# Performance work log

Measured on AMD Instinct MI355X. Metric: run time of the kernel, lower is better.

Reference implementation:

```python
import jax, jax.numpy as jnp
import numpy as np

TEMPERATURE = 0.1

def _l2norm(x):
    # F.normalize(dim=1) with eps clamp
    n = jnp.maximum(jnp.linalg.norm(x, axis=1, keepdims=True), 1e-12)
    return x / n

def _retrieval_metric(s):
    # T=1: position of the diagonal element in each row's descending sort.
    order = jnp.argsort(-s, axis=1)            # [N,N] descending argsort
    rankpos = jnp.argsort(order, axis=1)        # inverse permutation: rank of each column
    pos = jnp.diagonal(rankpos)                 # j such that rank[i][j] == i
    posf = pos.astype(s.dtype)
    r1 = jnp.mean((pos < 1).astype(s.dtype))
    r5 = jnp.mean((pos < 5).astype(s.dtype))
    r10 = jnp.mean((pos < 10).astype(s.dtype))
    mr = jnp.mean(posf)
    return r1, r5, r10, mr

def setup_inputs() -> dict:
    key = jax.random.key(0)
    k1, k2, k3, k4 = jax.random.split(key, 4)
    N, C = 4096, 512
    return {
        'v_feat': jax.random.normal(k1, (N, C), dtype=jnp.float32),
        't_feat': jax.random.normal(k2, (N, C), dtype=jnp.float32),
        'p_v': jax.random.normal(k3, (N, C), dtype=jnp.float32),
        'p_t': jax.random.normal(k4, (N, C), dtype=jnp.float32),
    }

def reference(v_feat, t_feat, p_v, p_t):
    vn = _l2norm(v_feat)
    tn = _l2norm(t_feat)
    pvn = _l2norm(p_v)
    ptn = _l2norm(p_t)
    sv = jnp.einsum('nc,mc->nm', vn, ptn) / TEMPERATURE  # [N,N]
    st = jnp.einsum('nc,mc->nm', tn, pvn) / TEMPERATURE  # [N,N]
    # nominator: scalar logsumexp over both diagonals (2N values)
    nominator = jax.nn.logsumexp(jnp.concatenate([jnp.diagonal(sv), jnp.diagonal(st)], axis=0))
    # denominator: per-row logsumexp over concatenated [N,2N]
    denominator = jax.nn.logsumexp(jnp.concatenate([sv, st], axis=1), axis=1)
    loss = jnp.mean(denominator - nominator)
    # metrics (no-grad path in original)
    v_std = jnp.mean(jnp.std(vn, axis=0, ddof=1))
    t_std = jnp.mean(jnp.std(tn, axis=0, ddof=1))
    pv_std = jnp.mean(jnp.std(pvn, axis=0, ddof=1))
    pt_std = jnp.mean(jnp.std(ptn, axis=0, ddof=1))
    sv_raw = jnp.einsum('nc,mc->nm', vn, ptn)
    st_raw = jnp.einsum('nc,mc->nm', tn, pvn)
    v_r1, v_r5, v_r10, v_mr = _retrieval_metric(sv_raw)
    t_r1, t_r5, t_r10, t_mr = _retrieval_metric(st_raw)
    return (loss, v_std, t_std, pv_std, pt_std,
            v_r1, v_r5, v_r10, v_mr,
            t_r1, t_r5, t_r10, t_mr)
```

## Files before the change

kernel.cpp:

```cpp
#include <hip/hip_runtime.h>
#include <hip/hip_bf16.h>

#define N 4096
#define C 512

typedef __attribute__((ext_vector_type(8))) short bf16x8;
typedef __attribute__((ext_vector_type(8))) short s16x8;
typedef __attribute__((ext_vector_type(4))) float f32x4;

__device__ inline float bf2f(__hip_bfloat16 h) { return __bfloat162float(h); }

__device__ inline void gload16(const void* g, void* l) {
    __builtin_amdgcn_global_load_lds(
        (__attribute__((address_space(1))) void*)(g),
        (__attribute__((address_space(3))) void*)(l),
        16, 0, 0);
}

__global__ __launch_bounds__(256) void k_prep(
    const float* __restrict__ s0, const float* __restrict__ s1f,
    const float* __restrict__ s2f, const float* __restrict__ s3,
    __hip_bfloat16* __restrict__ ws_hi0, long mat_stride,
    float* __restrict__ dv, float* __restrict__ dt,
    float* __restrict__ colsum, float* __restrict__ colsq)
{
    __shared__ float sa[4][512];
    __shared__ float sq[4][512];

    const int b = blockIdx.x;
    const int tid = threadIdx.x;
    const int lane = tid & 63;
    const int w = tid >> 6;

    const int pair = b >> 8;
    const int chunk = b & 255;
    const float* X = pair ? s1f : s0;
    const float* B = pair ? s2f : s3;
    const int mX = pair ? 1 : 0;
    const int mB = pair ? 2 : 3;
    __hip_bfloat16* hiX = ws_hi0 + (long)mX * mat_stride;
    __hip_bfloat16* loX = hiX + (long)N * C;
    __hip_bfloat16* hiB = ws_hi0 + (long)mB * mat_stride;
    __hip_bfloat16* loB = hiB + (long)N * C;
    float* dout = pair ? dt : dv;

    float aX[8], qX[8], aB[8], qB[8];
    for (int e = 0; e < 8; e++) { aX[e] = 0.f; qX[e] = 0.f; aB[e] = 0.f; qB[e] = 0.f; }

    const int row0 = chunk * 16 + w * 4;
    for (int i = 0; i < 4; i++) {
        const int row = row0 + i;
        const float4* x4 = (const float4*)(X + (size_t)row * C);
        const float4* b4 = (const float4*)(B + (size_t)row * C);
        float4 x0 = x4[lane * 2], x1 = x4[lane * 2 + 1];
        float4 b0 = b4[lane * 2], b1 = b4[lane * 2 + 1];

        float ss  = x0.x*x0.x + x0.y*x0.y + x0.z*x0.z + x0.w*x0.w
                  + x1.x*x1.x + x1.y*x1.y + x1.z*x1.z + x1.w*x1.w;
        float ssb = b0.x*b0.x + b0.y*b0.y + b0.z*b0.z + b0.w*b0.w
                  + b1.x*b1.x + b1.y*b1.y + b1.z*b1.z + b1.w*b1.w;
        float dot = x0.x*b0.x + x0.y*b0.y + x0.z*b0.z + x0.w*b0.w
                  + x1.x*b1.x + x1.y*b1.y + x1.z*b1.z + x1.w*b1.w;
        for (int o = 1; o < 64; o <<= 1) {
            ss  += __shfl_xor(ss, o);
            ssb += __shfl_xor(ssb, o);
            dot += __shfl_xor(dot, o);
        }
        float scX = 1.0f / fmaxf(sqrtf(ss), 1e-12f);
        float scB = 1.0f / fmaxf(sqrtf(ssb), 1e-12f);
        if (lane == 0) dout[row] = dot * scX * scB;

        float yx[8] = { x0.x*scX, x0.y*scX, x0.z*scX, x0.w*scX,
                        x1.x*scX, x1.y*scX, x1.z*scX, x1.w*scX };
        float yb[8] = { b0.x*scB, b0.y*scB, b0.z*scB, b0.w*scB,
                        b1.x*scB, b1.y*scB, b1.z*scB, b1.w*scB };
        __hip_bfloat16 hvx[8], lvx[8], hvb[8], lvb[8];
        for (int e = 0; e < 8; e++) {
            hvx[e] = __float2bfloat16(yx[e]);
            lvx[e] = __float2bfloat16(yx[e] - bf2f(hvx[e]));
            aX[e] += yx[e]; qX[e] += yx[e] * yx[e];
            hvb[e] = __float2bfloat16(yb[e]);
            lvb[e] = __float2bfloat16(yb[e] - bf2f(hvb[e]));
            aB[e] += yb[e]; qB[e] += yb[e] * yb[e];
        }
        size_t base = (size_t)row * C + lane * 8;
        *(s16x8*)(hiX + base) = *(s16x8*)hvx;
        *(s16x8*)(loX + base) = *(s16x8*)lvx;
        *(s16x8*)(hiB + base) = *(s16x8*)hvb;
        *(s16x8*)(loB + base) = *(s16x8*)lvb;
    }

    for (int e = 0; e < 8; e++) { sa[w][lane*8+e] = aX[e]; sq[w][lane*8+e] = qX[e]; }
    __syncthreads();
    for (int c = tid; c < 512; c += 256) {
        atomicAdd(&colsum[mX * 512 + c], sa[0][c] + sa[1][c] + sa[2][c] + sa[3][c]);
        atomicAdd(&colsq [mX * 512 + c], sq[0][c] + sq[1][c] + sq[2][c] + sq[3][c]);
    }
    __syncthreads();
    for (int e = 0; e < 8; e++) { sa[w][lane*8+e] = aB[e]; sq[w][lane*8+e] = qB[e]; }
    __syncthreads();
    for (int c = tid; c < 512; c += 256) {
        atomicAdd(&colsum[mB * 512 + c], sa[0][c] + sa[1][c] + sa[2][c] + sa[3][c]);
        atomicAdd(&colsq [mB * 512 + c], sq[0][c] + sq[1][c] + sq[2][c] + sq[3][c]);
    }
}

#define PLANE 8192
#define LIDX(BUF, ROW, COL) ((BUF) * PLANE + (ROW) * 32 + (COL))

__global__ __launch_bounds__(512, 2) void k_gemm(
    const __hip_bfloat16* __restrict__ h0, const __hip_bfloat16* __restrict__ l0,
    const __hip_bfloat16* __restrict__ h1, const __hip_bfloat16* __restrict__ l1,
    const __hip_bfloat16* __restrict__ h2, const __hip_bfloat16* __restrict__ l2,
    const __hip_bfloat16* __restrict__ h3, const __hip_bfloat16* __restrict__ l3,
    const float* __restrict__ dv, const float* __restrict__ dt,
    float* __restrict__ row_ev, float* __restrict__ row_et,
    float* __restrict__ row_cv, float* __restrict__ row_ct)
{
    __shared__ __align__(16) char smem[131072];
    __hip_bfloat16* SAh = (__hip_bfloat16*)smem;
    __hip_bfloat16* SAl = SAh + 2 * PLANE;
    __hip_bfloat16* SBh = SAh + 4 * PLANE;
    __hip_bfloat16* SBl = SAh + 6 * PLANE;

    const int z = blockIdx.z;
    const __hip_bfloat16* Ah = z ? h1 : h0;
    const __hip_bfloat16* Al = z ? l1 : l0;
    const __hip_bfloat16* Bh = z ? h2 : h3;
    const __hip_bfloat16* Bl = z ? l2 : l3;
    const float* diag = z ? dt : dv;
    float* row_e = z ? row_et : row_ev;
    float* row_c = z ? row_ct : row_cv;

    const int tid = threadIdx.x;
    const int lane = tid & 63;
    const int w = tid >> 6;
    const int wy = w >> 2, wx = w & 3;
    const int bm = blockIdx.x * 256;
    const int bn = blockIdx.y * 256;

    const int s0i = tid, s1i = tid + 512;
    const int r0 = s0i >> 2, q0 = s0i & 3;
    const int r1 = s1i >> 2, q1 = s1i & 3;
    const int g0 = (q0 ^ ((r0 >> 1) & 3)) * 8;
    const int g1 = (q1 ^ ((r1 >> 1) & 3)) * 8;
    const size_t aoff0 = (size_t)(bm + r0) * C + g0;
    const size_t aoff1 = (size_t)(bm + r1) * C + g1;
    const size_t boff0 = (size_t)(bn + r0) * C + g0;
    const size_t boff1 = (size_t)(bn + r1) * C + g1;
    const int d0 = s0i * 8, d1 = s1i * 8;

    const int fr = lane & 15;
    const int pcs = ((lane >> 4) ^ ((fr >> 1) & 3)) * 8;

    f32x4 acc[8][4];
    #pragma unroll
    for (int i = 0; i < 8; i++)
        #pragma unroll
        for (int j = 0; j < 4; j++)
            acc[i][j] = (f32x4){0.f, 0.f, 0.f, 0.f};

    gload16(Ah + aoff0, SAh + d0); gload16(Ah + aoff1, SAh + d1);
    gload16(Al + aoff0, SAl + d0); gload16(Al + aoff1, SAl + d1);
    gload16(Bh + boff0, SBh + d0); gload16(Bh + boff1, SBh + d1);
    gload16(Bl + boff0, SBl + d0); gload16(Bl + boff1, SBl + d1);
    __syncthreads();

#define MFMA1(d, a, b) d = __builtin_amdgcn_mfma_f32_16x16x32_bf16(a, b, d, 0, 0, 0)
#define QUAD(i0, i1, A0H, A0L, A1H, A1L) \
    MFMA1(acc[i0][0], A0H, bh[0]); MFMA1(acc[i0][1], A0H, bh[1]); \
    MFMA1(acc[i0][2], A0H, bh[2]); MFMA1(acc[i0][3], A0H, bh[3]); \
    MFMA1(acc[i1][0], A1H, bh[0]); MFMA1(acc[i1][1], A1H, bh[1]); \
    MFMA1(acc[i1][2], A1H, bh[2]); MFMA1(acc[i1][3], A1H, bh[3]); \
    MFMA1(acc[i0][0], A0H, bl[0]); MFMA1(acc[i0][1], A0H, bl[1]); \
    MFMA1(acc[i0][2], A0H, bl[2]); MFMA1(acc[i0][3], A0H, bl[3]); \
    MFMA1(acc[i1][0], A1H, bl[0]); MFMA1(acc[i1][1], A1H, bl[1]); \
    MFMA1(acc[i1][2], A1H, bl[2]); MFMA1(acc[i1][3], A1H, bl[3]); \
    MFMA1(acc[i0][0], A0L, bh[0]); MFMA1(acc[i0][1], A0L, bh[1]); \
    MFMA1(acc[i0][2], A0L, bh[2]); MFMA1(acc[i0][3], A0L, bh[3]); \
    MFMA1(acc[i1][0], A1L, bh[0]); MFMA1(acc[i1][1], A1L, bh[1]); \
    MFMA1(acc[i1][2], A1L, bh[2]); MFMA1(acc[i1][3], A1L, bh[3])

#define KBODY(RB, TCUR)                                                          \
    {                                                                            \
        const size_t kn = (size_t)((TCUR) + 1) * 32;                             \
        const int fpl = (1 - (RB)) * PLANE;                                      \
        const bool pf = ((TCUR) < NT - 1);                                       \
        bf16x8 bh[4], bl[4];                                                     \
        {             \
            if (pf) {                                                            \
                gload16(Ah + aoff0 + kn, SAh + fpl + d0);                        \
                gload16(Ah + aoff1 + kn, SAh + fpl + d1);                        \
                gload16(Al + aoff0 + kn, SAl + fpl + d0);                        \
                gload16(Al + aoff1 + kn, SAl + fpl + d1);                        \
            }                                                                    \
            _Pragma("unroll")                                                    \
            for (int j = 0; j < 4; j++) {                                        \
                bh[j] = *(const bf16x8*)&SBh[LIDX(RB, wx*64 + j*16 + fr, pcs)];  \
                bl[j] = *(const bf16x8*)&SBl[LIDX(RB, wx*64 + j*16 + fr, pcs)];  \
            }                                                                    \
            bf16x8 x0h = *(const bf16x8*)&SAh[LIDX(RB, wy*128 +   0 + fr, pcs)]; \
            bf16x8 x0l = *(const bf16x8*)&SAl[LIDX(RB, wy*128 +   0 + fr, pcs)]; \
            bf16x8 x1h = *(const bf16x8*)&SAh[LIDX(RB, wy*128 +  16 + fr, pcs)]; \
            bf16x8 x1l = *(const bf16x8*)&SAl[LIDX(RB, wy*128 +  16 + fr, pcs)]; \
            __builtin_amdgcn_s_setprio(1);                                       \
            QUAD(0, 1, x0h, x0l, x1h, x1l);                                      \
            __builtin_amdgcn_s_setprio(0);                                       \
        }                                                                        \
        {                       \
            if (pf) {                                                            \
                gload16(Bh + boff0 + kn, SBh + fpl + d0);                        \
                gload16(Bh + boff1 + kn, SBh + fpl + d1);                        \
                gload16(Bl + boff0 + kn, SBl + fpl + d0);                        \
                gload16(Bl + boff1 + kn, SBl + fpl + d1);                        \
            }                                                                    \
            bf16x8 x0h = *(const bf16x8*)&SAh[LIDX(RB, wy*128 +  32 + fr, pcs)]; \
            bf16x8 x0l = *(const bf16x8*)&SAl[LIDX(RB, wy*128 +  32 + fr, pcs)]; \
            bf16x8 x1h = *(const bf16x8*)&SAh[LIDX(RB, wy*128 +  48 + fr, pcs)]; \
            bf16x8 x1l = *(const bf16x8*)&SAl[LIDX(RB, wy*128 +  48 + fr, pcs)]; \
            __builtin_amdgcn_s_setprio(1);                                       \
            QUAD(2, 3, x0h, x0l, x1h, x1l);                                      \
            __builtin_amdgcn_s_setprio(0);                                       \
        }                                                                        \
        {                                            \
            bf16x8 x0h = *(const bf16x8*)&SAh[LIDX(RB, wy*128 +  64 + fr, pcs)]; \
            bf16x8 x0l = *(const bf16x8*)&SAl[LIDX(RB, wy*128 +  64 + fr, pcs)]; \
            bf16x8 x1h = *(const bf16x8*)&SAh[LIDX(RB, wy*128 +  80 + fr, pcs)]; \
            bf16x8 x1l = *(const bf16x8*)&SAl[LIDX(RB, wy*128 +  80 + fr, pcs)]; \
            __builtin_amdgcn_s_setprio(1);                                       \
            QUAD(4, 5, x0h, x0l, x1h, x1l);                                      \
            __builtin_amdgcn_s_setprio(0);                                       \
        }                                                                        \
        {    \
            bf16x8 x0h = *(const bf16x8*)&SAh[LIDX(RB, wy*128 +  96 + fr, pcs)]; \
            bf16x8 x0l = *(const bf16x8*)&SAl[LIDX(RB, wy*128 +  96 + fr, pcs)]; \
            bf16x8 x1h = *(const bf16x8*)&SAh[LIDX(RB, wy*128 + 112 + fr, pcs)]; \
            bf16x8 x1l = *(const bf16x8*)&SAl[LIDX(RB, wy*128 + 112 + fr, pcs)]; \
            __builtin_amdgcn_s_setprio(1);                                       \
            QUAD(6, 7, x0h, x0l, x1h, x1l);                                      \
            __builtin_amdgcn_s_setprio(0);                                       \
            __syncthreads();                                                     \
        }                                                                        \
    }

    const int NT = C / 32;
    #pragma unroll 1
    for (int tt = 0; tt < NT; tt += 2) {
        KBODY(0, tt)
        KBODY(1, tt + 1)
    }
#undef KBODY
#undef QUAD
#undef MFMA1

    float* sdiag = (float*)smem;
    float* sred  = (float*)(smem + 1024);
    if (tid < 256) sdiag[tid] = diag[bm + tid];
    __syncthreads();

    const int quad = lane >> 4;
    #pragma unroll
    for (int i = 0; i < 8; i++) {
        #pragma unroll
        for (int reg = 0; reg < 4; reg++) {
            const int rloc = wy * 128 + i * 16 + quad * 4 + reg;
            const int grow = bm + rloc;
            const float dgv = sdiag[rloc];
            float e = 0.f, cc = 0.f;
            #pragma unroll
            for (int j = 0; j < 4; j++) {
                float s = acc[i][j][reg];
                int gcol = bn + wx * 64 + j * 16 + fr;
                e += __expf(10.f * s - 10.f);
                if (s > dgv && gcol != grow) cc += 1.f;
            }
            for (int o = 1; o < 16; o <<= 1) {
                e += __shfl_xor(e, o);
                cc += __shfl_xor(cc, o);
            }
            if (fr == 0) {
                sred[(rloc * 4 + wx) * 2 + 0] = e;
                sred[(rloc * 4 + wx) * 2 + 1] = cc;
            }
        }
    }
    __syncthreads();
    if (tid < 256) {
        float se = 0.f, sc = 0.f;
        #pragma unroll
        for (int x = 0; x < 4; x++) {
            se += sred[(tid * 4 + x) * 2 + 0];
            sc += sred[(tid * 4 + x) * 2 + 1];
        }
        atomicAdd(&row_e[bm + tid], se);
        atomicAdd(&row_c[bm + tid], sc);
    }
}

__global__ __launch_bounds__(256) void k_fin(
    const float* __restrict__ dv, const float* __restrict__ dt,
    const float* __restrict__ row_ev, const float* __restrict__ row_et,
    const float* __restrict__ row_cv, const float* __restrict__ row_ct,
    const float* __restrict__ colsum, const float* __restrict__ colsq,
    float* __restrict__ out)
{
    const int t = threadIdx.x;
    const int lane = t & 63;
    const int wv = t >> 6;

    float vals[10];
    for (int k = 0; k < 10; k++) vals[k] = 0.f;
    for (int i = 0; i < 16; i++) {
        const int row = i * 256 + t;
        float se = row_ev[row] + row_et[row];
        float pv = row_cv[row];
        float pt = row_ct[row];
        vals[0] += logf(se) + 10.f;
        vals[1] += (pv < 0.5f) ? 1.f : 0.f;
        vals[2] += (pv < 4.5f) ? 1.f : 0.f;
        vals[3] += (pv < 9.5f) ? 1.f : 0.f;
        vals[4] += pv;
        vals[5] += (pt < 0.5f) ? 1.f : 0.f;
        vals[6] += (pt < 4.5f) ? 1.f : 0.f;
        vals[7] += (pt < 9.5f) ? 1.f : 0.f;
        vals[8] += pt;
        vals[9] += __expf(10.f * dv[row] - 10.f) + __expf(10.f * dt[row] - 10.f);
    }
    __shared__ float red[4][10];
    for (int k = 0; k < 10; k++) {
        float v = vals[k];
        for (int o = 1; o < 64; o <<= 1) v += __shfl_xor(v, o);
        if (lane == 0) red[wv][k] = v;
    }

    __shared__ float smat[4][4];
    for (int m = 0; m < 4; m++) {
        float sd2 = 0.f;
        for (int h = 0; h < 2; h++) {
            int c = h * 256 + t;
            float a = colsum[m * 512 + c];
            float q = colsq [m * 512 + c];
            float var = (q - a * a * (1.f / N)) * (1.f / (N - 1));
            sd2 += sqrtf(fmaxf(var, 0.f));
        }
        for (int o = 1; o < 64; o <<= 1) sd2 += __shfl_xor(sd2, o);
        if (lane == 0) smat[wv][m] = sd2;
    }
    __syncthreads();
    if (t == 0) {
        float g[10];
        for (int k = 0; k < 10; k++)
            g[k] = red[0][k] + red[1][k] + red[2][k] + red[3][k];
        float stds[4];
        for (int m = 0; m < 4; m++)
            stds[m] = (smat[0][m] + smat[1][m] + smat[2][m] + smat[3][m]) * (1.f / 512.f);
        const float invN = 1.f / N;
        float nominator = logf(g[9]) + 10.f;
        out[0]  = g[0] * invN - nominator;
        out[1]  = stds[0];
        out[2]  = stds[1];
        out[3]  = stds[2];
        out[4]  = stds[3];
        out[5]  = g[1] * invN;
        out[6]  = g[2] * invN;
        out[7]  = g[3] * invN;
        out[8]  = g[4] * invN;
        out[9]  = g[5] * invN;
        out[10] = g[6] * invN;
        out[11] = g[7] * invN;
        out[12] = g[8] * invN;
    }
}

extern "C" void kernel_launch(void* const* d_in, const int* in_sizes, int n_in,
                              void* d_out, int out_size, void* d_ws, size_t ws_size,
                              hipStream_t stream)
{
    char* p = (char*)d_ws;

    float* row_ev = (float*)p; p += N * 4;
    float* row_et = (float*)p; p += N * 4;
    float* row_cv = (float*)p; p += N * 4;
    float* row_ct = (float*)p; p += N * 4;
    float* colsum = (float*)p; p += 4 * 512 * 4;
    float* colsq  = (float*)p; p += 4 * 512 * 4;
    const size_t acc_bytes = (size_t)(p - (char*)d_ws);

    const size_t NE = (size_t)N * C;
    const long mat_stride = 2 * NE;
    __hip_bfloat16* hiA[4];
    __hip_bfloat16* loA[4];
    for (int m = 0; m < 4; m++) {
        hiA[m] = (__hip_bfloat16*)p; p += NE * 2;
        loA[m] = (__hip_bfloat16*)p; p += NE * 2;
    }
    float* dv = (float*)p; p += N * 4;
    float* dt = (float*)p; p += N * 4;

    hipMemsetAsync(d_ws, 0, acc_bytes, stream);

    k_prep<<<dim3(512), 256, 0, stream>>>(
        (const float*)d_in[0], (const float*)d_in[1],
        (const float*)d_in[2], (const float*)d_in[3],
        hiA[0], mat_stride, dv, dt, colsum, colsq);

    k_gemm<<<dim3(16, 16, 2), 512, 0, stream>>>(
        hiA[0], loA[0], hiA[1], loA[1], hiA[2], loA[2], hiA[3], loA[3],
        dv, dt, row_ev, row_et, row_cv, row_ct);

    k_fin<<<dim3(1), 256, 0, stream>>>(
        dv, dt, row_ev, row_et, row_cv, row_ct, colsum, colsq, (float*)d_out);
}
```

Before: 191.8 us.

## Fuse final reduction into GEMM via last-block counter and stagger wave MFMA order

Removes the separate single-block finalize kernel by having the last GEMM block, detected through an atomic counter, perform the final reductions and write the outputs. Odd waves process the A sub-tiles in a rotated order so that LDS reads are spread out across waves. The end-of-iteration __syncthreads is replaced with an explicit waitcnt, a raw barrier and a sched_barrier. This saves one kernel launch and its serialization gap, at the cost of a threadfence and an atomic per block, plus a serial tail inside the last block.

```diff
diff --git a/kernel.cpp b/kernel.cpp
--- a/kernel.cpp
+++ b/kernel.cpp
@@ -115,7 +115,9 @@
     const __hip_bfloat16* __restrict__ h3, const __hip_bfloat16* __restrict__ l3,
     const float* __restrict__ dv, const float* __restrict__ dt,
     float* __restrict__ row_ev, float* __restrict__ row_et,
-    float* __restrict__ row_cv, float* __restrict__ row_ct)
+    float* __restrict__ row_cv, float* __restrict__ row_ct,
+    const float* __restrict__ colsum, const float* __restrict__ colsq,
+    int* __restrict__ ctr, float* __restrict__ out)
 {
     __shared__ __align__(16) char smem[131072];
     __hip_bfloat16* SAh = (__hip_bfloat16*)smem;
@@ -181,13 +183,13 @@
     MFMA1(acc[i1][0], A1L, bh[0]); MFMA1(acc[i1][1], A1L, bh[1]); \
     MFMA1(acc[i1][2], A1L, bh[2]); MFMA1(acc[i1][3], A1L, bh[3])
 
-#define KBODY(RB, TCUR)                                                          \
+#define KBODY(RB, TCUR, P0A, P0B, P1A, P1B, P2A, P2B, P3A, P3B)                  \
     {                                                                            \
         const size_t kn = (size_t)((TCUR) + 1) * 32;                             \
         const int fpl = (1 - (RB)) * PLANE;                                      \
         const bool pf = ((TCUR) < NT - 1);                                       \
         bf16x8 bh[4], bl[4];                                                     \
-        {             \
+        {           \
             if (pf) {                                                            \
                 gload16(Ah + aoff0 + kn, SAh + fpl + d0);                        \
                 gload16(Ah + aoff1 + kn, SAh + fpl + d1);                        \
@@ -199,55 +201,63 @@
                 bh[j] = *(const bf16x8*)&SBh[LIDX(RB, wx*64 + j*16 + fr, pcs)];  \
                 bl[j] = *(const bf16x8*)&SBl[LIDX(RB, wx*64 + j*16 + fr, pcs)];  \
             }                                                                    \
-            bf16x8 x0h = *(const bf16x8*)&SAh[LIDX(RB, wy*128 +   0 + fr, pcs)]; \
-            bf16x8 x0l = *(const bf16x8*)&SAl[LIDX(RB, wy*128 +   0 + fr, pcs)]; \
-            bf16x8 x1h = *(const bf16x8*)&SAh[LIDX(RB, wy*128 +  16 + fr, pcs)]; \
-            bf16x8 x1l = *(const bf16x8*)&SAl[LIDX(RB, wy*128 +  16 + fr, pcs)]; \
+            bf16x8 x0h = *(const bf16x8*)&SAh[LIDX(RB, wy*128 + (P0A)*16 + fr, pcs)]; \
+            bf16x8 x0l = *(const bf16x8*)&SAl[LIDX(RB, wy*128 + (P0A)*16 + fr, pcs)]; \
+            bf16x8 x1h = *(const bf16x8*)&SAh[LIDX(RB, wy*128 + (P0B)*16 + fr, pcs)]; \
+            bf16x8 x1l = *(const bf16x8*)&SAl[LIDX(RB, wy*128 + (P0B)*16 + fr, pcs)]; \
             __builtin_amdgcn_s_setprio(1);                                       \
-            QUAD(0, 1, x0h, x0l, x1h, x1l);                                      \
+            QUAD(P0A, P0B, x0h, x0l, x1h, x1l);                                  \
             __builtin_amdgcn_s_setprio(0);                                       \
         }                                                                        \
-        {                       \
+        {                    \
             if (pf) {                                                            \
                 gload16(Bh + boff0 + kn, SBh + fpl + d0);                        \
                 gload16(Bh + boff1 + kn, SBh + fpl + d1);                        \
                 gload16(Bl + boff0 + kn, SBl + fpl + d0);                        \
                 gload16(Bl + boff1 + kn, SBl + fpl + d1);                        \
             }                                                                    \
-            bf16x8 x0h = *(const bf16x8*)&SAh[LIDX(RB, wy*128 +  32 + fr, pcs)]; \
-            bf16x8 x0l = *(const bf16x8*)&SAl[LIDX(RB, wy*128 +  32 + fr, pcs)]; \
-            bf16x8 x1h = *(const bf16x8*)&SAh[LIDX(RB, wy*128 +  48 + fr, pcs)]; \
-            bf16x8 x1l = *(const bf16x8*)&SAl[LIDX(RB, wy*128 +  48 + fr, pcs)]; \
+            bf16x8 x0h = *(const bf16x8*)&SAh[LIDX(RB, wy*128 + (P1A)*16 + fr, pcs)]; \
+            bf16x8 x0l = *(const bf16x8*)&SAl[LIDX(RB, wy*128 + (P1A)*16 + fr, pcs)]; \
+            bf16x8 x1h = *(const bf16x8*)&SAh[LIDX(RB, wy*128 + (P1B)*16 + fr, pcs)]; \
+            bf16x8 x1l = *(const bf16x8*)&SAl[LIDX(RB, wy*128 + (P1B)*16 + fr, pcs)]; \
             __builtin_amdgcn_s_setprio(1);                                       \
-            QUAD(2, 3, x0h, x0l, x1h, x1l);                                      \
+            QUAD(P1A, P1B, x0h, x0l, x1h, x1l);                                  \
             __builtin_amdgcn_s_setprio(0);                                       \
         }                                                                        \
-        {                                            \
-            bf16x8 x0h = *(const bf16x8*)&SAh[LIDX(RB, wy*128 +  64 + fr, pcs)]; \
-            bf16x8 x0l = *(const bf16x8*)&SAl[LIDX(RB, wy*128 +  64 + fr, pcs)]; \
-            bf16x8 x1h = *(const bf16x8*)&SAh[LIDX(RB, wy*128 +  80 + fr, pcs)]; \
-            bf16x8 x1l = *(const bf16x8*)&SAl[LIDX(RB, wy*128 +  80 + fr, pcs)]; \
+        {                                          \
+            bf16x8 x0h = *(const bf16x8*)&SAh[LIDX(RB, wy*128 + (P2A)*16 + fr, pcs)]; \
+            bf16x8 x0l = *(const bf16x8*)&SAl[LIDX(RB, wy*128 + (P2A)*16 + fr, pcs)]; \
+            bf16x8 x1h = *(const bf16x8*)&SAh[LIDX(RB, wy*128 + (P2B)*16 + fr, pcs)]; \
+            bf16x8 x1l = *(const bf16x8*)&SAl[LIDX(RB, wy*128 + (P2B)*16 + fr, pcs)]; \
             __builtin_amdgcn_s_setprio(1);                                       \
-            QUAD(4, 5, x0h, x0l, x1h, x1l);                                      \
+            QUAD(P2A, P2B, x0h, x0l, x1h, x1l);                                  \
             __builtin_amdgcn_s_setprio(0);                                       \
         }                                                                        \
-        {    \
-            bf16x8 x0h = *(const bf16x8*)&SAh[LIDX(RB, wy*128 +  96 + fr, pcs)]; \
-            bf16x8 x0l = *(const bf16x8*)&SAl[LIDX(RB, wy*128 +  96 + fr, pcs)]; \
-            bf16x8 x1h = *(const bf16x8*)&SAh[LIDX(RB, wy*128 + 112 + fr, pcs)]; \
-            bf16x8 x1l = *(const bf16x8*)&SAl[LIDX(RB, wy*128 + 112 + fr, pcs)]; \
+        {        \
+            bf16x8 x0h = *(const bf16x8*)&SAh[LIDX(RB, wy*128 + (P3A)*16 + fr, pcs)]; \
+            bf16x8 x0l = *(const bf16x8*)&SAl[LIDX(RB, wy*128 + (P3A)*16 + fr, pcs)]; \
+            bf16x8 x1h = *(const bf16x8*)&SAh[LIDX(RB, wy*128 + (P3B)*16 + fr, pcs)]; \
+            bf16x8 x1l = *(const bf16x8*)&SAl[LIDX(RB, wy*128 + (P3B)*16 + fr, pcs)]; \
             __builtin_amdgcn_s_setprio(1);                                       \
-            QUAD(6, 7, x0h, x0l, x1h, x1l);                                      \
+            QUAD(P3A, P3B, x0h, x0l, x1h, x1l);                                  \
             __builtin_amdgcn_s_setprio(0);                                       \
-            __syncthreads();                                                     \
+            asm volatile("s_waitcnt vmcnt(0) lgkmcnt(0)" ::: "memory");          \
+            __builtin_amdgcn_s_barrier();                                        \
+            __builtin_amdgcn_sched_barrier(0);                                   \
         }                                                                        \
     }
 
     const int NT = C / 32;
+    const bool wodd = (w & 1) != 0;
     #pragma unroll 1
     for (int tt = 0; tt < NT; tt += 2) {
-        KBODY(0, tt)
-        KBODY(1, tt + 1)
+        if (!wodd) {
+            KBODY(0, tt,     0, 1, 2, 3, 4, 5, 6, 7)
+            KBODY(1, tt + 1, 0, 1, 2, 3, 4, 5, 6, 7)
+        } else {
+            KBODY(0, tt,     4, 5, 6, 7, 0, 1, 2, 3)
+            KBODY(1, tt + 1, 4, 5, 6, 7, 0, 1, 2, 3)
+        }
     }
 #undef KBODY
 #undef QUAD
@@ -295,80 +305,81 @@
         atomicAdd(&row_e[bm + tid], se);
         atomicAdd(&row_c[bm + tid], sc);
     }
-}
-
-__global__ __launch_bounds__(256) void k_fin(
-    const float* __restrict__ dv, const float* __restrict__ dt,
-    const float* __restrict__ row_ev, const float* __restrict__ row_et,
-    const float* __restrict__ row_cv, const float* __restrict__ row_ct,
-    const float* __restrict__ colsum, const float* __restrict__ colsq,
-    float* __restrict__ out)
-{
-    const int t = threadIdx.x;
-    const int lane = t & 63;
-    const int wv = t >> 6;
-
-    float vals[10];
-    for (int k = 0; k < 10; k++) vals[k] = 0.f;
-    for (int i = 0; i < 16; i++) {
-        const int row = i * 256 + t;
-        float se = row_ev[row] + row_et[row];
-        float pv = row_cv[row];
-        float pt = row_ct[row];
-        vals[0] += logf(se) + 10.f;
-        vals[1] += (pv < 0.5f) ? 1.f : 0.f;
-        vals[2] += (pv < 4.5f) ? 1.f : 0.f;
-        vals[3] += (pv < 9.5f) ? 1.f : 0.f;
-        vals[4] += pv;
-        vals[5] += (pt < 0.5f) ? 1.f : 0.f;
-        vals[6] += (pt < 4.5f) ? 1.f : 0.f;
-        vals[7] += (pt < 9.5f) ? 1.f : 0.f;
-        vals[8] += pt;
-        vals[9] += __expf(10.f * dv[row] - 10.f) + __expf(10.f * dt[row] - 10.f);
-    }
-    __shared__ float red[4][10];
-    for (int k = 0; k < 10; k++) {
-        float v = vals[k];
-        for (int o = 1; o < 64; o <<= 1) v += __shfl_xor(v, o);
-        if (lane == 0) red[wv][k] = v;
-    }
-
-    __shared__ float smat[4][4];
-    for (int m = 0; m < 4; m++) {
-        float sd2 = 0.f;
-        for (int h = 0; h < 2; h++) {
-            int c = h * 256 + t;
-            float a = colsum[m * 512 + c];
-            float q = colsq [m * 512 + c];
+
+    __threadfence();
+    __syncthreads();
+    volatile int* lastflag = (volatile int*)(smem + 12288);
+    if (tid == 0) {
+        int old = atomicAdd(ctr, 1);
+        *lastflag = (old == 511) ? 1 : 0;
+    }
+    __syncthreads();
+    if (*lastflag) {
+        __threadfence();
+        float vals[10];
+        #pragma unroll
+        for (int k = 0; k < 10; k++) vals[k] = 0.f;
+        for (int i = 0; i < 8; i++) {
+            const int row = i * 512 + tid;
+            float se = atomicAdd(&row_ev[row], 0.f) + atomicAdd(&row_et[row], 0.f);
+            float pv = atomicAdd(&row_cv[row], 0.f);
+            float pt = atomicAdd(&row_ct[row], 0.f);
+            vals[0] += logf(se) + 10.f;
+            vals[1] += (pv < 0.5f) ? 1.f : 0.f;
+            vals[2] += (pv < 4.5f) ? 1.f : 0.f;
+            vals[3] += (pv < 9.5f) ? 1.f : 0.f;
+            vals[4] += pv;
+            vals[5] += (pt < 0.5f) ? 1.f : 0.f;
+            vals[6] += (pt < 4.5f) ? 1.f : 0.f;
+            vals[7] += (pt < 9.5f) ? 1.f : 0.f;
+            vals[8] += pt;
+            vals[9] += __expf(10.f * dv[row] - 10.f) + __expf(10.f * dt[row] - 10.f);
+        }
+        float* fred = (float*)smem;
+        for (int k = 0; k < 10; k++) {
+            float v = vals[k];
+            for (int o = 1; o < 64; o <<= 1) v += __shfl_xor(v, o);
+            if (lane == 0) fred[w * 10 + k] = v;
+        }
+        float* fmat = (float*)(smem + 512);
+        for (int m = 0; m < 4; m++) {
+            float a = colsum[m * 512 + tid];
+            float q = colsq [m * 512 + tid];
             float var = (q - a * a * (1.f / N)) * (1.f / (N - 1));
-            sd2 += sqrtf(fmaxf(var, 0.f));
-        }
-        for (int o = 1; o < 64; o <<= 1) sd2 += __shfl_xor(sd2, o);
-        if (lane == 0) smat[wv][m] = sd2;
-    }
-    __syncthreads();
-    if (t == 0) {
-        float g[10];
-        for (int k = 0; k < 10; k++)
-            g[k] = red[0][k] + red[1][k] + red[2][k] + red[3][k];
-        float stds[4];
-        for (int m = 0; m < 4; m++)
-            stds[m] = (smat[0][m] + smat[1][m] + smat[2][m] + smat[3][m]) * (1.f / 512.f);
-        const float invN = 1.f / N;
-        float nominator = logf(g[9]) + 10.f;
-        out[0]  = g[0] * invN - nominator;
-        out[1]  = stds[0];
-        out[2]  = stds[1];
-        out[3]  = stds[2];
-        out[4]  = stds[3];
-        out[5]  = g[1] * invN;
-        out[6]  = g[2] * invN;
-        out[7]  = g[3] * invN;
-        out[8]  = g[4] * invN;
-        out[9]  = g[5] * invN;
-        out[10] = g[6] * invN;
-        out[11] = g[7] * invN;
-        out[12] = g[8] * invN;
+            float sd = sqrtf(fmaxf(var, 0.f));
+            for (int o = 1; o < 64; o <<= 1) sd += __shfl_xor(sd, o);
+            if (lane == 0) fmat[w * 4 + m] = sd;
+        }
+        __syncthreads();
+        if (tid == 0) {
+            float g[10];
+            for (int k = 0; k < 10; k++) {
+                float s = 0.f;
+                for (int wq = 0; wq < 8; wq++) s += fred[wq * 10 + k];
+                g[k] = s;
+            }
+            float stds[4];
+            for (int m = 0; m < 4; m++) {
+                float s = 0.f;
+                for (int wq = 0; wq < 8; wq++) s += fmat[wq * 4 + m];
+                stds[m] = s * (1.f / 512.f);
+            }
+            const float invN = 1.f / N;
+            float nominator = logf(g[9]) + 10.f;
+            out[0]  = g[0] * invN - nominator;
+            out[1]  = stds[0];
+            out[2]  = stds[1];
+            out[3]  = stds[2];
+            out[4]  = stds[3];
+            out[5]  = g[1] * invN;
+            out[6]  = g[2] * invN;
+            out[7]  = g[3] * invN;
+            out[8]  = g[4] * invN;
+            out[9]  = g[5] * invN;
+            out[10] = g[6] * invN;
+            out[11] = g[7] * invN;
+            out[12] = g[8] * invN;
+        }
     }
 }
 
@@ -384,6 +395,7 @@
     float* row_ct = (float*)p; p += N * 4;
     float* colsum = (float*)p; p += 4 * 512 * 4;
     float* colsq  = (float*)p; p += 4 * 512 * 4;
+    int*   ctr    = (int*)p;   p += 16;
     const size_t acc_bytes = (size_t)(p - (char*)d_ws);
 
     const size_t NE = (size_t)N * C;
@@ -406,8 +418,6 @@
 
     k_gemm<<<dim3(16, 16, 2), 512, 0, stream>>>(
         hiA[0], loA[0], hiA[1], loA[1], hiA[2], loA[2], hiA[3], loA[3],
-        dv, dt, row_ev, row_et, row_cv, row_ct);
-
-    k_fin<<<dim3(1), 256, 0, stream>>>(
-        dv, dt, row_ev, row_et, row_cv, row_ct, colsum, colsq, (float*)d_out);
+        dv, dt, row_ev, row_et, row_cv, row_ct,
+        colsum, colsq, ctr, (float*)d_out);
 }
```

Result: slower. 257.0 us (+34.0%).

## Use 1024-thread GEMM blocks with smaller per-wave 64x64 output tiles

Applied to the files above, without the earlier changes.

Doubles the k_gemm block from 8 to 16 waves while keeping the 256x256 block tile. Each wave now accumulates a 64x64 sub-tile instead of 128x64, and each thread issues one global-to-LDS load per matrix per stage instead of two. The goal is more waves per CU to hide LDS and MFMA latency, since the 128KB LDS footprint already limits the CU to one block. The cost is less register-level reuse of the A fragments, more LDS reads per MFMA, and a tighter register budget under __launch_bounds__(1024,4), which could cause spills.

```diff
diff --git a/kernel.cpp b/kernel.cpp
--- a/kernel.cpp
+++ b/kernel.cpp
@@ -108,7 +108,7 @@
 #define PLANE 8192
 #define LIDX(BUF, ROW, COL) ((BUF) * PLANE + (ROW) * 32 + (COL))
 
-__global__ __launch_bounds__(512, 2) void k_gemm(
+__global__ __launch_bounds__(1024, 4) void k_gemm(
     const __hip_bfloat16* __restrict__ h0, const __hip_bfloat16* __restrict__ l0,
     const __hip_bfloat16* __restrict__ h1, const __hip_bfloat16* __restrict__ l1,
     const __hip_bfloat16* __restrict__ h2, const __hip_bfloat16* __restrict__ l2,
@@ -139,47 +139,36 @@
     const int bm = blockIdx.x * 256;
     const int bn = blockIdx.y * 256;
 
-    const int s0i = tid, s1i = tid + 512;
-    const int r0 = s0i >> 2, q0 = s0i & 3;
-    const int r1 = s1i >> 2, q1 = s1i & 3;
+    const int r0 = tid >> 2, q0 = tid & 3;
     const int g0 = (q0 ^ ((r0 >> 1) & 3)) * 8;
-    const int g1 = (q1 ^ ((r1 >> 1) & 3)) * 8;
     const size_t aoff0 = (size_t)(bm + r0) * C + g0;
-    const size_t aoff1 = (size_t)(bm + r1) * C + g1;
     const size_t boff0 = (size_t)(bn + r0) * C + g0;
-    const size_t boff1 = (size_t)(bn + r1) * C + g1;
-    const int d0 = s0i * 8, d1 = s1i * 8;
+    const int d0 = tid * 8;
 
     const int fr = lane & 15;
     const int pcs = ((lane >> 4) ^ ((fr >> 1) & 3)) * 8;
 
-    f32x4 acc[8][4];
+    f32x4 acc[4][4];
     #pragma unroll
-    for (int i = 0; i < 8; i++)
+    for (int i = 0; i < 4; i++)
         #pragma unroll
         for (int j = 0; j < 4; j++)
             acc[i][j] = (f32x4){0.f, 0.f, 0.f, 0.f};
 
-    gload16(Ah + aoff0, SAh + d0); gload16(Ah + aoff1, SAh + d1);
-    gload16(Al + aoff0, SAl + d0); gload16(Al + aoff1, SAl + d1);
-    gload16(Bh + boff0, SBh + d0); gload16(Bh + boff1, SBh + d1);
-    gload16(Bl + boff0, SBl + d0); gload16(Bl + boff1, SBl + d1);
+    gload16(Ah + aoff0, SAh + d0);
+    gload16(Al + aoff0, SAl + d0);
+    gload16(Bh + boff0, SBh + d0);
+    gload16(Bl + boff0, SBl + d0);
     __syncthreads();
 
 #define MFMA1(d, a, b) d = __builtin_amdgcn_mfma_f32_16x16x32_bf16(a, b, d, 0, 0, 0)
-#define QUAD(i0, i1, A0H, A0L, A1H, A1L) \
-    MFMA1(acc[i0][0], A0H, bh[0]); MFMA1(acc[i0][1], A0H, bh[1]); \
-    MFMA1(acc[i0][2], A0H, bh[2]); MFMA1(acc[i0][3], A0H, bh[3]); \
-    MFMA1(acc[i1][0], A1H, bh[0]); MFMA1(acc[i1][1], A1H, bh[1]); \
-    MFMA1(acc[i1][2], A1H, bh[2]); MFMA1(acc[i1][3], A1H, bh[3]); \
-    MFMA1(acc[i0][0], A0H, bl[0]); MFMA1(acc[i0][1], A0H, bl[1]); \
-    MFMA1(acc[i0][2], A0H, bl[2]); MFMA1(acc[i0][3], A0H, bl[3]); \
-    MFMA1(acc[i1][0], A1H, bl[0]); MFMA1(acc[i1][1], A1H, bl[1]); \
-    MFMA1(acc[i1][2], A1H, bl[2]); MFMA1(acc[i1][3], A1H, bl[3]); \
-    MFMA1(acc[i0][0], A0L, bh[0]); MFMA1(acc[i0][1], A0L, bh[1]); \
-    MFMA1(acc[i0][2], A0L, bh[2]); MFMA1(acc[i0][3], A0L, bh[3]); \
-    MFMA1(acc[i1][0], A1L, bh[0]); MFMA1(acc[i1][1], A1L, bh[1]); \
-    MFMA1(acc[i1][2], A1L, bh[2]); MFMA1(acc[i1][3], A1L, bh[3])
+#define TRIO(I, XH, XL) \
+    MFMA1(acc[I][0], XH, bh[0]); MFMA1(acc[I][1], XH, bh[1]); \
+    MFMA1(acc[I][2], XH, bh[2]); MFMA1(acc[I][3], XH, bh[3]); \
+    MFMA1(acc[I][0], XH, bl[0]); MFMA1(acc[I][1], XH, bl[1]); \
+    MFMA1(acc[I][2], XH, bl[2]); MFMA1(acc[I][3], XH, bl[3]); \
+    MFMA1(acc[I][0], XL, bh[0]); MFMA1(acc[I][1], XL, bh[1]); \
+    MFMA1(acc[I][2], XL, bh[2]); MFMA1(acc[I][3], XL, bh[3])
 
 #define KBODY(RB, TCUR)                                                          \
     {                                                                            \
@@ -187,57 +176,43 @@
         const int fpl = (1 - (RB)) * PLANE;                                      \
         const bool pf = ((TCUR) < NT - 1);                                       \
         bf16x8 bh[4], bl[4];                                                     \
-        {             \
+        {            \
             if (pf) {                                                            \
                 gload16(Ah + aoff0 + kn, SAh + fpl + d0);                        \
-                gload16(Ah + aoff1 + kn, SAh + fpl + d1);                        \
                 gload16(Al + aoff0 + kn, SAl + fpl + d0);                        \
-                gload16(Al + aoff1 + kn, SAl + fpl + d1);                        \
+                gload16(Bh + boff0 + kn, SBh + fpl + d0);                        \
+                gload16(Bl + boff0 + kn, SBl + fpl + d0);                        \
             }                                                                    \
             _Pragma("unroll")                                                    \
             for (int j = 0; j < 4; j++) {                                        \
                 bh[j] = *(const bf16x8*)&SBh[LIDX(RB, wx*64 + j*16 + fr, pcs)];  \
                 bl[j] = *(const bf16x8*)&SBl[LIDX(RB, wx*64 + j*16 + fr, pcs)];  \
             }                                                                    \
-            bf16x8 x0h = *(const bf16x8*)&SAh[LIDX(RB, wy*128 +   0 + fr, pcs)]; \
-            bf16x8 x0l = *(const bf16x8*)&SAl[LIDX(RB, wy*128 +   0 + fr, pcs)]; \
-            bf16x8 x1h = *(const bf16x8*)&SAh[LIDX(RB, wy*128 +  16 + fr, pcs)]; \
-            bf16x8 x1l = *(const bf16x8*)&SAl[LIDX(RB, wy*128 +  16 + fr, pcs)]; \
+            bf16x8 xh = *(const bf16x8*)&SAh[LIDX(RB, wy*64 +  0 + fr, pcs)];    \
+            bf16x8 xl = *(const bf16x8*)&SAl[LIDX(RB, wy*64 +  0 + fr, pcs)];    \
             __builtin_amdgcn_s_setprio(1);                                       \
-            QUAD(0, 1, x0h, x0l, x1h, x1l);                                      \
-            __builtin_amdgcn_s_setprio(0);                                       \
-        }                                                                        \
-        {                       \
-            if (pf) {                                                            \
-                gload16(Bh + boff0 + kn, SBh + fpl + d0);                        \
-                gload16(Bh + boff1 + kn, SBh + fpl + d1);                        \
-                gload16(Bl + boff0 + kn, SBl + fpl + d0);                        \
-                gload16(Bl + boff1 + kn, SBl + fpl + d1);                        \
-            }                                                                    \
-            bf16x8 x0h = *(const bf16x8*)&SAh[LIDX(RB, wy*128 +  32 + fr, pcs)]; \
-            bf16x8 x0l = *(const bf16x8*)&SAl[LIDX(RB, wy*128 +  32 + fr, pcs)]; \
-            bf16x8 x1h = *(const bf16x8*)&SAh[LIDX(RB, wy*128 +  48 + fr, pcs)]; \
-            bf16x8 x1l = *(const bf16x8*)&SAl[LIDX(RB, wy*128 +  48 + fr, pcs)]; \
-            __builtin_amdgcn_s_setprio(1);                                       \
-            QUAD(2, 3, x0h, x0l, x1h, x1l);                                      \
+            TRIO(0, xh, xl);                                                     \
             __builtin_amdgcn_s_setprio(0);                                       \
         }                                                                        \
         {                                            \
-            bf16x8 x0h = *(const bf16x8*)&SAh[LIDX(RB, wy*128 +  64 + fr, pcs)]; \
-            bf16x8 x0l = *(const bf16x8*)&SAl[LIDX(RB, wy*128 +  64 + fr, pcs)]; \
-            bf16x8 x1h = *(const bf16x8*)&SAh[LIDX(RB, wy*128 +  80 + fr, pcs)]; \
-            bf16x8 x1l = *(const bf16x8*)&SAl[LIDX(RB, wy*128 +  80 + fr, pcs)]; \
+            bf16x8 xh = *(const bf16x8*)&SAh[LIDX(RB, wy*64 + 16 + fr, pcs)];    \
+            bf16x8 xl = *(const bf16x8*)&SAl[LIDX(RB, wy*64 + 16 + fr, pcs)];    \
             __builtin_amdgcn_s_setprio(1);                                       \
-            QUAD(4, 5, x0h, x0l, x1h, x1l);                                      \
+            TRIO(1, xh, xl);                                                     \
+            __builtin_amdgcn_s_setprio(0);                                       \
+        }                                                                        \
+        {                                            \
+            bf16x8 xh = *(const bf16x8*)&SAh[LIDX(RB, wy*64 + 32 + fr, pcs)];    \
+            bf16x8 xl = *(const bf16x8*)&SAl[LIDX(RB, wy*64 + 32 + fr, pcs)];    \
+            __builtin_amdgcn_s_setprio(1);                                       \
+            TRIO(2, xh, xl);                                                     \
             __builtin_amdgcn_s_setprio(0);                                       \
         }                                                                        \
         {    \
-            bf16x8 x0h = *(const bf16x8*)&SAh[LIDX(RB, wy*128 +  96 + fr, pcs)]; \
-            bf16x8 x0l = *(const bf16x8*)&SAl[LIDX(RB, wy*128 +  96 + fr, pcs)]; \
-            bf16x8 x1h = *(const bf16x8*)&SAh[LIDX(RB, wy*128 + 112 + fr, pcs)]; \
-            bf16x8 x1l = *(const bf16x8*)&SAl[LIDX(RB, wy*128 + 112 + fr, pcs)]; \
+            bf16x8 xh = *(const bf16x8*)&SAh[LIDX(RB, wy*64 + 48 + fr, pcs)];    \
+            bf16x8 xl = *(const bf16x8*)&SAl[LIDX(RB, wy*64 + 48 + fr, pcs)];    \
             __builtin_amdgcn_s_setprio(1);                                       \
-            QUAD(6, 7, x0h, x0l, x1h, x1l);                                      \
+            TRIO(3, xh, xl);                                                     \
             __builtin_amdgcn_s_setprio(0);                                       \
             __syncthreads();                                                     \
         }                                                                        \
@@ -250,7 +225,7 @@
         KBODY(1, tt + 1)
     }
 #undef KBODY
-#undef QUAD
+#undef TRIO
 #undef MFMA1
 
     float* sdiag = (float*)smem;
@@ -260,10 +235,10 @@
 
     const int quad = lane >> 4;
     #pragma unroll
-    for (int i = 0; i < 8; i++) {
+    for (int i = 0; i < 4; i++) {
         #pragma unroll
         for (int reg = 0; reg < 4; reg++) {
-            const int rloc = wy * 128 + i * 16 + quad * 4 + reg;
+            const int rloc = wy * 64 + i * 16 + quad * 4 + reg;
             const int grow = bm + rloc;
             const float dgv = sdiag[rloc];
             float e = 0.f, cc = 0.f;
@@ -404,7 +379,7 @@
         (const float*)d_in[2], (const float*)d_in[3],
         hiA[0], mat_stride, dv, dt, colsum, colsq);
 
-    k_gemm<<<dim3(16, 16, 2), 512, 0, stream>>>(
+    k_gemm<<<dim3(16, 16, 2), 1024, 0, stream>>>(
         hiA[0], loA[0], hiA[1], loA[1], hiA[2], loA[2], hiA[3], loA[3],
         dv, dt, row_ev, row_et, row_cv, row_ct);
 
```

After: 264.2 us. 1.38x slower.
